# Kernel tuning notes

Hardware: AMD Instinct MI355X
Metric: run time of the kernel (lower is better)

## Reference

```python
import jax, jax.numpy as jnp
import numpy as np

B, T = 128, 512
V, D = 50000, 128
LSTM_SIZE = 256
H = LSTM_SIZE // 2  # per-direction hidden = 128
K = 32              # num_tags


def setup_inputs() -> dict:
    key = jax.random.key(0)
    ks = jax.random.split(key, 16)
    s = 0.05
    inputs = jax.random.randint(ks[0], (B, T), 0, V, dtype=jnp.int32)
    tags = jax.random.randint(ks[1], (B, T), 0, K, dtype=jnp.int32)
    emb = (jax.random.normal(ks[2], (V, D)) * s).at[0].set(0.0)  # padding_idx=0
    # LSTM params, PyTorch gate order [i,f,g,o]; dim0 of stacks = [fwd, bwd]
    w_ih_l0 = jax.random.normal(ks[3], (2, 4 * H, D)) * s
    w_hh_l0 = jax.random.normal(ks[4], (2, 4 * H, H)) * s
    b_l0 = jax.random.normal(ks[5], (2, 4 * H)) * s  # b_ih + b_hh combined
    w_ih_l1 = jax.random.normal(ks[6], (2, 4 * H, 2 * H)) * s
    w_hh_l1 = jax.random.normal(ks[7], (2, 4 * H, H)) * s
    b_l1 = jax.random.normal(ks[8], (2, 4 * H)) * s
    W_out = jax.random.normal(ks[9], (K, 2 * H)) * s
    b_out = jax.random.normal(ks[10], (K,)) * s
    start_t = jax.random.normal(ks[11], (K,)) * s
    end_t = jax.random.normal(ks[12], (K,)) * s
    trans = jax.random.normal(ks[13], (K, K)) * s
    return {"inputs": inputs, "tags": tags, "emb": emb,
            "w_ih_l0": w_ih_l0, "w_hh_l0": w_hh_l0, "b_l0": b_l0,
            "w_ih_l1": w_ih_l1, "w_hh_l1": w_hh_l1, "b_l1": b_l1,
            "W_out": W_out, "b_out": b_out,
            "start_t": start_t, "end_t": end_t, "trans": trans}


def _lstm_dir(xT, Wih, Whh, b, reverse):
    # xT: [T,B,Din] time-major
    Bn = xT.shape[1]
    Hn = Whh.shape[1]

    def step(carry, xt):
        h, c = carry
        z = xt @ Wih.T + h @ Whh.T + b  # [B,4H]
        i, f, g, o = jnp.split(z, 4, axis=-1)
        c = jax.nn.sigmoid(f) * c + jax.nn.sigmoid(i) * jnp.tanh(g)
        h = jax.nn.sigmoid(o) * jnp.tanh(c)
        return (h, c), h

    init = (jnp.zeros((Bn, Hn), xT.dtype), jnp.zeros((Bn, Hn), xT.dtype))
    _, hs = jax.lax.scan(step, init, xT, reverse=reverse)
    return hs  # [T,B,H], in original time order


def _bilstm_layer(xT, w_ih, w_hh, b):
    hf = _lstm_dir(xT, w_ih[0], w_hh[0], b[0], False)
    hb = _lstm_dir(xT, w_ih[1], w_hh[1], b[1], True)
    return jnp.concatenate([hf, hb], axis=-1)  # [T,B,2H]


def _viterbi(emT, start_t, end_t, trans):
    # emT: [T,B,K] time-major emissions; returns [B,T] int32 best tags
    score0 = start_t[None, :] + emT[0]  # [B,K]

    def step(score, em_t):
        # cand[b,i,j] = score[b,i] + trans[i,j] + em_t[b,j]
        cand = score[:, :, None] + trans[None] + em_t[:, None, :]
        return jnp.max(cand, axis=1), jnp.argmax(cand, axis=1).astype(jnp.int32)

    score, hist = jax.lax.scan(step, score0, emT[1:])  # hist: [T-1,B,K]
    score = score + end_t[None, :]
    last = jnp.argmax(score, axis=-1).astype(jnp.int32)  # [B]

    def back(tag, hist_t):
        prev = jnp.take_along_axis(hist_t, tag[:, None], axis=1)[:, 0]
        return prev, prev

    _, prevs = jax.lax.scan(back, last, hist, reverse=True)  # [T-1,B]
    return jnp.concatenate([prevs, last[None]], axis=0).T  # [B,T]


def reference(inputs, tags, emb, w_ih_l0, w_hh_l0, b_l0,
              w_ih_l1, w_hh_l1, b_l1, W_out, b_out,
              start_t, end_t, trans):
    # Embedding lookup -> time-major
    x = emb[inputs]                      # [B,T,D]
    xT = jnp.transpose(x, (1, 0, 2))     # [T,B,D]
    h1 = _bilstm_layer(xT, w_ih_l0, w_hh_l0, b_l0)   # [T,B,2H] (dropout is eval no-op)
    h2 = _bilstm_layer(h1, w_ih_l1, w_hh_l1, b_l1)   # [T,B,2H]
    emT = h2 @ W_out.T + b_out           # [T,B,K]
    return _viterbi(emT, start_t, end_t, trans)      # [B,T] int32
```

## Files before the change

### kernel.cpp

```cpp
#include <hip/hip_runtime.h>
#include <cmath>

static constexpr int NB   = 128;
static constexpr int NT   = 512;
static constexpr int ND   = 128;
static constexpr int NH   = 128;
static constexpr int NG4  = 512;
static constexpr int NKT  = 32;
static constexpr int CHUNK = 128;
static constexpr int NCH  = NT / CHUNK;

__device__ __forceinline__ float sigf(float x) { return 1.0f / (1.0f + expf(-x)); }

__global__ __launch_bounds__(256) void prep_w(
    const float* __restrict__ W, float* __restrict__ wt, int DIN)
{
    const int KT = DIN >> 4;
    const int o = blockIdx.x * 256 + threadIdx.x;
    const int j  = o & 255;
    const int k  = (o >> 8) & 15;
    const int cb = o >> 12;
    const int kt = cb % KT;
    const int dct = cb / KT;
    const int d  = dct >> 1;
    const int ct = dct & 1;
    wt[o] = W[(size_t)(d * 512 + ct * 256 + j) * DIN + kt * 16 + k];
}

template <int DIN>
__device__ __forceinline__ void proj_body(
    const float* __restrict__ wt,
    const float* __restrict__ bias,
    const float* __restrict__ xsrc,
    const int*   __restrict__ inputs,
    float*       __restrict__ zin,
    int c)
{
    constexpr int KT = DIN / 16;
    __shared__ __align__(16) float A[2][16][128];
    __shared__ __align__(16) float Bs[2][16][256];
    __shared__ const float* rowp[128];

    const int bid = blockIdx.x;
    const int d  = bid >> 8;
    const int b  = (bid >> 1) & 127;
    const int ct = bid & 1;
    const int tid = threadIdx.x;
    const int tx = tid & 31;
    const int ty = tid >> 5;
    const int q  = tid & 3;
    const int r0 = tid >> 2;

    if (tid < 128) {
        const int s = tid;
        const int ttl = c * CHUNK + s;
        const int t = d ? (NT - 1 - ttl) : ttl;
        if constexpr (DIN == 128) {
            rowp[tid] = xsrc + (size_t)inputs[b * NT + t] * ND;
        } else {
            rowp[tid] = xsrc + ((size_t)(b * NT + t)) * 256;
        }
    }
    __syncthreads();

    const float* rp0 = rowp[r0];
    const float* rp1 = rowp[r0 + 64];
    const float* wtb = wt + ((size_t)(d * 2 + ct)) * KT * 4096;

    float acc[16][8];
#pragma unroll
    for (int i = 0; i < 16; ++i)
#pragma unroll
        for (int n = 0; n < 8; ++n) acc[i][n] = 0.0f;

    float4 pa0 = *(const float4*)(rp0 + q * 4);
    float4 pa1 = *(const float4*)(rp1 + q * 4);
    float4 pb0 = ((const float4*)wtb)[tid];
    float4 pb1 = ((const float4*)wtb)[tid + 256];
    float4 pb2 = ((const float4*)wtb)[tid + 512];
    float4 pb3 = ((const float4*)wtb)[tid + 768];

    for (int kt = 0; kt < KT; ++kt) {
        const int buf = kt & 1;
        A[buf][q * 4 + 0][r0] = pa0.x; A[buf][q * 4 + 1][r0] = pa0.y;
        A[buf][q * 4 + 2][r0] = pa0.z; A[buf][q * 4 + 3][r0] = pa0.w;
        A[buf][q * 4 + 0][r0 + 64] = pa1.x; A[buf][q * 4 + 1][r0 + 64] = pa1.y;
        A[buf][q * 4 + 2][r0 + 64] = pa1.z; A[buf][q * 4 + 3][r0 + 64] = pa1.w;
        {
            const int e0 = tid;        *(float4*)&Bs[buf][e0 >> 6][(e0 & 63) * 4] = pb0;
            const int e1 = tid + 256;  *(float4*)&Bs[buf][e1 >> 6][(e1 & 63) * 4] = pb1;
            const int e2 = tid + 512;  *(float4*)&Bs[buf][e2 >> 6][(e2 & 63) * 4] = pb2;
            const int e3 = tid + 768;  *(float4*)&Bs[buf][e3 >> 6][(e3 & 63) * 4] = pb3;
        }
        __syncthreads();

        if (kt + 1 < KT) {
            const int k0 = (kt + 1) * 16;
            pa0 = *(const float4*)(rp0 + k0 + q * 4);
            pa1 = *(const float4*)(rp1 + k0 + q * 4);
            const float4* wkt = (const float4*)(wtb + (size_t)(kt + 1) * 4096);
            pb0 = wkt[tid];
            pb1 = wkt[tid + 256];
            pb2 = wkt[tid + 512];
            pb3 = wkt[tid + 768];
        }

#pragma unroll 2
        for (int k = 0; k < 16; ++k) {
            float4 a0 = *(const float4*)&A[buf][k][ty * 16];
            float4 a1 = *(const float4*)&A[buf][k][ty * 16 + 4];
            float4 a2 = *(const float4*)&A[buf][k][ty * 16 + 8];
            float4 a3 = *(const float4*)&A[buf][k][ty * 16 + 12];
            float4 b0 = *(const float4*)&Bs[buf][k][tx * 4];
            float4 b1 = *(const float4*)&Bs[buf][k][128 + tx * 4];
            const float ar[16] = {a0.x, a0.y, a0.z, a0.w, a1.x, a1.y, a1.z, a1.w,
                                  a2.x, a2.y, a2.z, a2.w, a3.x, a3.y, a3.z, a3.w};
            const float br[8]  = {b0.x, b0.y, b0.z, b0.w, b1.x, b1.y, b1.z, b1.w};
#pragma unroll
            for (int i = 0; i < 16; ++i)
#pragma unroll
                for (int n = 0; n < 8; ++n) acc[i][n] += ar[i] * br[n];
        }
    }

    float4 bb0 = *(const float4*)(bias + d * NG4 + ct * 256 + tx * 4);
    float4 bb1 = *(const float4*)(bias + d * NG4 + ct * 256 + 128 + tx * 4);
#pragma unroll
    for (int i = 0; i < 16; ++i) {
        const int s = ty * 16 + i;
        float* zp = zin + (((size_t)(d * NB + b) * CHUNK + s)) * NG4 + ct * 256;
        float4 o0, o1;
        o0.x = acc[i][0] + bb0.x; o0.y = acc[i][1] + bb0.y;
        o0.z = acc[i][2] + bb0.z; o0.w = acc[i][3] + bb0.w;
        o1.x = acc[i][4] + bb1.x; o1.y = acc[i][5] + bb1.y;
        o1.z = acc[i][6] + bb1.z; o1.w = acc[i][7] + bb1.w;
        *(float4*)(zp + tx * 4) = o0;
        *(float4*)(zp + 128 + tx * 4) = o1;
    }
}

__global__ __launch_bounds__(256) void proj_l0(
    const float* __restrict__ wt, const float* __restrict__ bias,
    const float* __restrict__ xsrc, const int* __restrict__ inputs,
    float* __restrict__ zin, int c)
{ proj_body<128>(wt, bias, xsrc, inputs, zin, c); }

__global__ __launch_bounds__(256) void proj_l1(
    const float* __restrict__ wt, const float* __restrict__ bias,
    const float* __restrict__ xsrc, const int* __restrict__ inputs,
    float* __restrict__ zin, int c)
{ proj_body<256>(wt, bias, xsrc, inputs, zin, c); }

__global__ __launch_bounds__(1024, 4) void lstm_rec_kernel(
    const float* __restrict__ Whh,
    const float* __restrict__ zin,
    float*       __restrict__ hout,
    float*       __restrict__ state_h,
    float*       __restrict__ state_c,
    int c)
{
    __shared__ __align__(16) float h_lds[128];
    __shared__ float p_lds[1024];

    const int bid = blockIdx.x;
    const int d = bid >> 7, b = bid & 127;
    const int tid = threadIdx.x;
    const int j = tid & 511, q = tid >> 9;

    float w[64];
    const float* wrow = Whh + ((size_t)(d * NG4 + j)) * NH + q * 64;
#pragma unroll
    for (int kk = 0; kk < 64; kk += 4) {
        float4 t4 = *(const float4*)(wrow + kk);
        w[kk] = t4.x; w[kk + 1] = t4.y; w[kk + 2] = t4.z; w[kk + 3] = t4.w;
    }
#pragma unroll
    for (int kk = 0; kk < 64; ++kk) {
        asm volatile("" : "+v"(w[kk]));
    }

    float c_reg = 0.0f;
    if (tid < 128) {
        float h0 = 0.0f;
        if (c != 0) {
            h0    = state_h[(d * NB + b) * NH + tid];
            c_reg = state_c[(d * NB + b) * NH + tid];
        }
        h_lds[tid] = h0;
    }
    __syncthreads();

    const float* zb = zin + ((size_t)(d * NB + b)) * CHUNK * NG4;

    for (int s = 0; s < CHUNK; ++s) {
        float z0 = 0.f, z1 = 0.f, z2 = 0.f, z3 = 0.f;
        if (tid < 128) {
            const float* zr = zb + (size_t)s * NG4;
            z0 = zr[tid]; z1 = zr[128 + tid]; z2 = zr[256 + tid]; z3 = zr[384 + tid];
        }
        float acc = 0.0f;
        const float* hp = h_lds + q * 64;
#pragma unroll
        for (int kk = 0; kk < 64; kk += 4) {
            float4 hv = *(const float4*)(hp + kk);
            acc += w[kk] * hv.x + w[kk + 1] * hv.y + w[kk + 2] * hv.z + w[kk + 3] * hv.w;
        }
        p_lds[tid] = acc;
        __syncthreads();

        if (tid < 128) {
            const float zi = z0 + p_lds[tid]       + p_lds[512 + tid];
            const float zf = z1 + p_lds[128 + tid] + p_lds[640 + tid];
            const float zg = z2 + p_lds[256 + tid] + p_lds[768 + tid];
            const float zo = z3 + p_lds[384 + tid] + p_lds[896 + tid];
            const float ig = sigf(zi), fg = sigf(zf), og = sigf(zo);
            c_reg = fg * c_reg + ig * tanhf(zg);
            const float hn = og * tanhf(c_reg);
            const int ttl = c * CHUNK + s;
            const int t   = d ? (NT - 1 - ttl) : ttl;
            h_lds[tid] = hn;
            hout[((size_t)(b * NT + t)) * 256 + d * NH + tid] = hn;
        }
        __syncthreads();
    }

    if (tid < 128) {
        state_h[(d * NB + b) * NH + tid] = h_lds[tid];
        state_c[(d * NB + b) * NH + tid] = c_reg;
    }
}

__global__ __launch_bounds__(256) void emis_kernel(
    const float* __restrict__ h2,
    const float* __restrict__ Wout,
    const float* __restrict__ bout,
    float*       __restrict__ em)
{
    __shared__ float wt[256 * 32];
    __shared__ __align__(16) float hrow[8][256];

    const int tid = threadIdx.x;
    const int k = tid & 31;
    const int rl = tid >> 5;

    for (int e = tid; e < 8192; e += 256) {
        const int kk = e >> 8, cc = e & 255;
        wt[cc * 32 + kk] = Wout[e];
    }
    const float bk = bout[k];
    __syncthreads();

    const size_t base = (size_t)blockIdx.x * 64;
    for (int rr = 0; rr < 8; ++rr) {
        const size_t r0 = base + rr * 8;
        for (int e = tid; e < 512; e += 256) {
            ((float4*)&hrow[0][0])[e] = ((const float4*)(h2 + r0 * 256))[e];
        }
        __syncthreads();
        float acc = bk;
#pragma unroll 8
        for (int cc = 0; cc < 256; cc += 4) {
            float4 hv = *(const float4*)&hrow[rl][cc];
            acc += hv.x * wt[cc * 32 + k] + hv.y * wt[(cc + 1) * 32 + k] +
                   hv.z * wt[(cc + 2) * 32 + k] + hv.w * wt[(cc + 3) * 32 + k];
        }
        em[(r0 + rl) * NKT + k] = acc;
        __syncthreads();
    }
}

__global__ __launch_bounds__(64) void viterbi_nb(
    const float* __restrict__ em,
    const float* __restrict__ start_t,
    const float* __restrict__ end_t,
    const float* __restrict__ trans,
    int*         __restrict__ out)
{
    __shared__ float score[32];
    __shared__ float tr[1024];
    __shared__ float fsc[32];
    __shared__ unsigned char hist[(NT - 1) * 32];

    const int b = blockIdx.x;
    const int lane = threadIdx.x;
    const int j = lane & 31, h = lane >> 5;

    for (int e = lane; e < 1024; e += 64) tr[e] = trans[e];
    const float* emb_ = em + (size_t)b * NT * NKT;
    if (lane < 32) score[j] = start_t[j] + emb_[j];
    __syncthreads();

    float em_next = emb_[NKT + j];
    for (int t = 1; t < NT; ++t) {
        const float em_j = em_next;
        if (t + 1 < NT) em_next = emb_[(size_t)(t + 1) * NKT + j];
        float best = -1e30f;
        int bi = 0;
#pragma unroll
        for (int ii = 0; ii < 16; ++ii) {
            const int i = h * 16 + ii;
            const float v = (score[i] + tr[i * 32 + j]) + em_j;
            if (v > best) { best = v; bi = i; }
        }
        const float ob  = __shfl(best, lane ^ 32);
        const int   obi = __shfl(bi,   lane ^ 32);
        if (h == 0) {
            float ns; int arg;
            if (ob > best) { ns = ob; arg = obi; }
            else           { ns = best; arg = bi; }
            score[j] = ns;
            hist[(t - 1) * 32 + j] = (unsigned char)arg;
        }
    }

    if (lane < 32) fsc[j] = score[j] + end_t[j];
    if (lane == 0) {
        float best = -1e30f; int bi = 0;
        for (int i = 0; i < 32; ++i) {
            const float v = fsc[i];
            if (v > best) { best = v; bi = i; }
        }
        int tag = bi;
        out[b * NT + (NT - 1)] = tag;
        for (int t = NT - 2; t >= 0; --t) {
            tag = hist[t * 32 + tag];
            out[b * NT + t] = tag;
        }
    }
}

extern "C" void kernel_launch(void* const* d_in, const int* in_sizes, int n_in,
                              void* d_out, int out_size, void* d_ws, size_t ws_size,
                              hipStream_t stream) {
    const int*   inputs  = (const int*)d_in[0];
    const float* emb     = (const float*)d_in[2];
    const float* w_ih_l0 = (const float*)d_in[3];
    const float* w_hh_l0 = (const float*)d_in[4];
    const float* b_l0    = (const float*)d_in[5];
    const float* w_ih_l1 = (const float*)d_in[6];
    const float* w_hh_l1 = (const float*)d_in[7];
    const float* b_l1    = (const float*)d_in[8];
    const float* W_out   = (const float*)d_in[9];
    const float* b_out   = (const float*)d_in[10];
    const float* start_t = (const float*)d_in[11];
    const float* end_t   = (const float*)d_in[12];
    const float* trans   = (const float*)d_in[13];
    int* out = (int*)d_out;

    float* ws  = (float*)d_ws;
    float* zin = ws;
    float* h1  = zin + (size_t)2 * NB * CHUNK * NG4;
    float* h2  = h1 + (size_t)NB * NT * 256;
    float* sth = h2 + (size_t)NB * NT * 256;
    float* stc = sth + (size_t)2 * NB * NH;
    float* em  = stc + (size_t)2 * NB * NH;
    float* wt0 = em + (size_t)NB * NT * NKT;
    float* wt1 = wt0 + (size_t)2 * 512 * 128;

    prep_w<<<512, 256, 0, stream>>>(w_ih_l0, wt0, 128);
    prep_w<<<1024, 256, 0, stream>>>(w_ih_l1, wt1, 256);

    for (int c = 0; c < NCH; ++c) {
        proj_l0<<<512, 256, 0, stream>>>(wt0, b_l0, emb, inputs, zin, c);
        lstm_rec_kernel<<<256, 1024, 0, stream>>>(w_hh_l0, zin, h1, sth, stc, c);
    }
    for (int c = 0; c < NCH; ++c) {
        proj_l1<<<512, 256, 0, stream>>>(wt1, b_l1, h1, nullptr, zin, c);
        lstm_rec_kernel<<<256, 1024, 0, stream>>>(w_hh_l1, zin, h2, sth, stc, c);
    }
    emis_kernel<<<(NB * NT) / 64, 256, 0, stream>>>(h2, W_out, b_out, em);
    viterbi_nb<<<NB, 64, 0, stream>>>(em, start_t, end_t, trans, out);
}
```

Before: 2.027 ms.

## Split LSTM recurrence across four waves with 256 weights per thread

The recurrent LSTM kernel now runs 256 threads per block instead of 1024. Each wave owns a 32-wide K slice and each lane computes eight gate rows, keeping 256 weight values in registers. Partial sums from the four waves are reduced through LDS. This cuts barrier participants and LDS h-reads per step, but raises register pressure sharply and leaves only four waves per block to hide latency.

```diff
diff --git a/kernel.cpp b/kernel.cpp
--- a/kernel.cpp
+++ b/kernel.cpp
@@ -151,7 +151,7 @@
     float* __restrict__ zin, int c)
 { proj_body<256>(wt, bias, xsrc, inputs, zin, c); }
 
-__global__ __launch_bounds__(1024, 4) void lstm_rec_kernel(
+__global__ __launch_bounds__(256, 1) void lstm_rec_ks(
     const float* __restrict__ Whh,
     const float* __restrict__ zin,
     float*       __restrict__ hout,
@@ -160,24 +160,29 @@
     int c)
 {
     __shared__ __align__(16) float h_lds[128];
-    __shared__ float p_lds[1024];
+    __shared__ __align__(16) float p_lds[4][512];
 
     const int bid = blockIdx.x;
     const int d = bid >> 7, b = bid & 127;
     const int tid = threadIdx.x;
-    const int j = tid & 511, q = tid >> 9;
-
-    float w[64];
-    const float* wrow = Whh + ((size_t)(d * NG4 + j)) * NH + q * 64;
-#pragma unroll
-    for (int kk = 0; kk < 64; kk += 4) {
-        float4 t4 = *(const float4*)(wrow + kk);
-        w[kk] = t4.x; w[kk + 1] = t4.y; w[kk + 2] = t4.z; w[kk + 3] = t4.w;
-    }
-#pragma unroll
-    for (int kk = 0; kk < 64; ++kk) {
-        asm volatile("" : "+v"(w[kk]));
-    }
+    const int wv = tid >> 6;
+    const int l  = tid & 63;
+
+    float w[8][32];
+#pragma unroll
+    for (int i = 0; i < 8; ++i) {
+        const float* wr = Whh + ((size_t)(d * NG4 + l + 64 * i)) * NH + wv * 32;
+#pragma unroll
+        for (int kk = 0; kk < 32; kk += 4) {
+            float4 t4 = *(const float4*)(wr + kk);
+            w[i][kk] = t4.x; w[i][kk + 1] = t4.y; w[i][kk + 2] = t4.z; w[i][kk + 3] = t4.w;
+        }
+    }
+#pragma unroll
+    for (int i = 0; i < 8; ++i)
+#pragma unroll
+        for (int kk = 0; kk < 32; ++kk)
+            asm volatile("" : "+v"(w[i][kk]));
 
     float c_reg = 0.0f;
     if (tid < 128) {
@@ -198,21 +203,32 @@
             const float* zr = zb + (size_t)s * NG4;
             z0 = zr[tid]; z1 = zr[128 + tid]; z2 = zr[256 + tid]; z3 = zr[384 + tid];
         }
-        float acc = 0.0f;
-        const float* hp = h_lds + q * 64;
-#pragma unroll
-        for (int kk = 0; kk < 64; kk += 4) {
-            float4 hv = *(const float4*)(hp + kk);
-            acc += w[kk] * hv.x + w[kk + 1] * hv.y + w[kk + 2] * hv.z + w[kk + 3] * hv.w;
-        }
-        p_lds[tid] = acc;
+
+        float hv[32];
+        const float* hp = h_lds + wv * 32;
+#pragma unroll
+        for (int kk = 0; kk < 32; kk += 4) {
+            float4 t4 = *(const float4*)(hp + kk);
+            hv[kk] = t4.x; hv[kk + 1] = t4.y; hv[kk + 2] = t4.z; hv[kk + 3] = t4.w;
+        }
+#pragma unroll
+        for (int i = 0; i < 8; ++i) {
+            float a = 0.0f;
+#pragma unroll
+            for (int kk = 0; kk < 32; ++kk) a += w[i][kk] * hv[kk];
+            p_lds[wv][l + 64 * i] = a;
+        }
         __syncthreads();
 
         if (tid < 128) {
-            const float zi = z0 + p_lds[tid]       + p_lds[512 + tid];
-            const float zf = z1 + p_lds[128 + tid] + p_lds[640 + tid];
-            const float zg = z2 + p_lds[256 + tid] + p_lds[768 + tid];
-            const float zo = z3 + p_lds[384 + tid] + p_lds[896 + tid];
+            const float si = (p_lds[0][tid] + p_lds[1][tid]) + (p_lds[2][tid] + p_lds[3][tid]);
+            const float sf = (p_lds[0][128 + tid] + p_lds[1][128 + tid]) + (p_lds[2][128 + tid] + p_lds[3][128 + tid]);
+            const float sg = (p_lds[0][256 + tid] + p_lds[1][256 + tid]) + (p_lds[2][256 + tid] + p_lds[3][256 + tid]);
+            const float so = (p_lds[0][384 + tid] + p_lds[1][384 + tid]) + (p_lds[2][384 + tid] + p_lds[3][384 + tid]);
+            const float zi = z0 + si;
+            const float zf = z1 + sf;
+            const float zg = z2 + sg;
+            const float zo = z3 + so;
             const float ig = sigf(zi), fg = sigf(zf), og = sigf(zo);
             c_reg = fg * c_reg + ig * tanhf(zg);
             const float hn = og * tanhf(c_reg);
@@ -362,11 +378,11 @@
 
     for (int c = 0; c < NCH; ++c) {
         proj_l0<<<512, 256, 0, stream>>>(wt0, b_l0, emb, inputs, zin, c);
-        lstm_rec_kernel<<<256, 1024, 0, stream>>>(w_hh_l0, zin, h1, sth, stc, c);
+        lstm_rec_ks<<<256, 256, 0, stream>>>(w_hh_l0, zin, h1, sth, stc, c);
     }
     for (int c = 0; c < NCH; ++c) {
         proj_l1<<<512, 256, 0, stream>>>(wt1, b_l1, h1, nullptr, zin, c);
-        lstm_rec_kernel<<<256, 1024, 0, stream>>>(w_hh_l1, zin, h2, sth, stc, c);
+        lstm_rec_ks<<<256, 256, 0, stream>>>(w_hh_l1, zin, h2, sth, stc, c);
     }
     emis_kernel<<<(NB * NT) / 64, 256, 0, stream>>>(h2, W_out, b_out, em);
     viterbi_nb<<<NB, 64, 0, stream>>>(em, start_t, end_t, trans, out);
```

Result: slower. 2.224 ms (+9.8%).
